# Performance work log

Measured on AMD Instinct MI355X. Metric: run time of the kernel, lower is better.

Reference implementation:

```python
import jax, jax.numpy as jnp
import numpy as np

D_MODEL = 1024
N_HEADS = 16
D_K = D_MODEL // N_HEADS

def setup_inputs() -> dict:
    key = jax.random.key(0)
    ks = jax.random.split(key, 11)
    B, S = 2, 2048
    s = 1.0 / np.sqrt(D_MODEL)
    inp = {
        'Q': jax.random.normal(ks[0], (B, S, D_MODEL), jnp.float32),
        'K': jax.random.normal(ks[1], (B, S, D_MODEL), jnp.float32),
        'V': jax.random.normal(ks[2], (B, S, D_MODEL), jnp.float32),
        'Wq': jax.random.normal(ks[3], (D_MODEL, D_MODEL), jnp.float32) * s,
        'bq': jnp.zeros((D_MODEL,), jnp.float32),
        'Wk': jax.random.normal(ks[4], (D_MODEL, D_MODEL), jnp.float32) * s,
        'bk': jnp.zeros((D_MODEL,), jnp.float32),
        'Wv': jax.random.normal(ks[5], (D_MODEL, D_MODEL), jnp.float32) * s,
        'bv': jnp.zeros((D_MODEL,), jnp.float32),
        'Wo': jax.random.normal(ks[6], (D_MODEL, D_MODEL), jnp.float32) * s,
        'bo': jnp.zeros((D_MODEL,), jnp.float32),
    }
    return inp

def _split_heads(x):
    B, S, _ = x.shape
    return x.reshape(B, S, N_HEADS, D_K).transpose(0, 2, 1, 3)  # [B,H,S,dk]

def reference(Q, K, V, Wq, bq, Wk, bk, Wv, bv, Wo, bo):
    q = _split_heads(Q @ Wq.T + bq)
    k = _split_heads(K @ Wk.T + bk)
    v = _split_heads(V @ Wv.T + bv)
    scores = jnp.einsum('bhqd,bhkd->bhqk', q, k) / jnp.sqrt(jnp.asarray(D_K, q.dtype))
    attn_weights = jax.nn.softmax(scores, axis=-1)          # [B,H,S,S]
    attn_out = jnp.einsum('bhqk,bhkd->bhqd', attn_weights, v)
    B, H, S, dk = attn_out.shape
    attn_out = attn_out.transpose(0, 2, 1, 3).reshape(B, S, H * dk)
    out = attn_out @ Wo.T + bo
    return (out, attn_weights)
```

## Files before the change

kernel.cpp:

```cpp
#include <hip/hip_runtime.h>
#include <hip/hip_bf16.h>
#include <math.h>


typedef __bf16 bf16;
typedef __bf16 bf16x8 __attribute__((ext_vector_type(8)));
typedef float  f32x4  __attribute__((ext_vector_type(4)));

#define GLDS16(gp, lp) __builtin_amdgcn_global_load_lds(                     \
    (const __attribute__((address_space(1))) void*)(gp),                     \
    (__attribute__((address_space(3))) void*)(lp), 16, 0, 0)

#define QSCALE 0.18033688011112042f

static __device__ __forceinline__ bf16x8 cvt8(const f32x4 lo, const f32x4 hi) {
    bf16x8 r;
    r[0] = (bf16)lo[0]; r[1] = (bf16)lo[1]; r[2] = (bf16)lo[2]; r[3] = (bf16)lo[3];
    r[4] = (bf16)hi[0]; r[5] = (bf16)hi[1]; r[6] = (bf16)hi[2]; r[7] = (bf16)hi[3];
    return r;
}

__global__ __launch_bounds__(256)
void cvt7(const float* __restrict__ s0, const float* __restrict__ s1, const float* __restrict__ s2,
          const float* __restrict__ s3, const float* __restrict__ s4, const float* __restrict__ s5,
          const float* __restrict__ s6,
          bf16* __restrict__ d0, bf16* __restrict__ d1, bf16* __restrict__ d2,
          bf16* __restrict__ d3, bf16* __restrict__ d4, bf16* __restrict__ d5,
          bf16* __restrict__ d6)
{
    const int seg = blockIdx.y;
    const float* s; bf16* d; int n;
    switch (seg) {
        case 0: s = s0; d = d0; n = 4194304; break;
        case 1: s = s1; d = d1; n = 4194304; break;
        case 2: s = s2; d = d2; n = 4194304; break;
        case 3: s = s3; d = d3; n = 1048576; break;
        case 4: s = s4; d = d4; n = 1048576; break;
        case 5: s = s5; d = d5; n = 1048576; break;
        default: s = s6; d = d6; n = 1048576; break;
    }
    const size_t i = ((size_t)blockIdx.x * 256 + threadIdx.x) * 8;
    if (i >= (size_t)n) return;
    const f32x4 lo = *(const f32x4*)(s + i);
    const f32x4 hi = *(const f32x4*)(s + i + 4);
    *(bf16x8*)(d + i) = cvt8(lo, hi);
}

template<int MODE>
__global__ __launch_bounds__(256)
void gemm_bb(const bf16* __restrict__ A0, const bf16* __restrict__ A1, const bf16* __restrict__ A2,
             const bf16* __restrict__ W0, const bf16* __restrict__ W1, const bf16* __restrict__ W2,
             const float* __restrict__ B0, const float* __restrict__ B1, const float* __restrict__ B2,
             void* __restrict__ O0v, void* __restrict__ O1v, void* __restrict__ O2v)
{
    __shared__ __align__(16) bf16 As[128 * 32];
    __shared__ __align__(16) bf16 Bs[128 * 32];

    const int tid  = threadIdx.x;
    const int lane = tid & 63;
    const int w    = tid >> 6;
    const int wr   = w >> 1, wc = w & 1;
    const int g    = lane >> 4, c = lane & 15;

    const int mb  = blockIdx.x, nb = blockIdx.y;
    const int mat = (MODE == 1) ? (nb >> 3) : 0;
    const int nbi = (MODE == 1) ? (nb & 7) : nb;

    const bf16*  A  = (MODE == 1) ? (mat == 0 ? A0 : (mat == 1 ? A1 : A2)) : A0;
    const bf16*  W  = (MODE == 1) ? (mat == 0 ? W0 : (mat == 1 ? W1 : W2)) : W0;
    const float* Bi = (MODE == 1) ? (mat == 0 ? B0 : (mat == 1 ? B1 : B2)) : B0;

    const size_t m0 = (size_t)mb * 128;
    const int    n0 = nbi * 128;

    f32x4 acc[4][4];
#pragma unroll
    for (int i = 0; i < 4; i++)
#pragma unroll
        for (int j = 0; j < 4; j++) acc[i][j] = (f32x4){0.f, 0.f, 0.f, 0.f};

    const int srow = lane >> 2;
    const int spos = lane & 3;

    for (int k0 = 0; k0 < 1024; k0 += 32) {
        __syncthreads();
#pragma unroll
        for (int s = 0; s < 2; s++) {
            const int ca  = w * 2 + s;
            const int row = ca * 16 + srow;
            GLDS16(A + (size_t)(m0 + row) * 1024 + k0 + ((spos ^ ((row >> 1) & 3)) << 3),
                   &As[ca * 512]);
            GLDS16(W + (size_t)(n0 + row) * 1024 + k0 + ((spos ^ ((row >> 1) & 3)) << 3),
                   &Bs[ca * 512]);
        }
        __syncthreads();

        bf16x8 av[4], bv[4];
#pragma unroll
        for (int i = 0; i < 4; i++) {
            const int row = wr * 64 + i * 16 + c;
            av[i] = *(const bf16x8*)&As[row * 32 + ((g ^ ((row >> 1) & 3)) << 3)];
        }
#pragma unroll
        for (int j = 0; j < 4; j++) {
            const int row = wc * 64 + j * 16 + c;
            bv[j] = *(const bf16x8*)&Bs[row * 32 + ((g ^ ((row >> 1) & 3)) << 3)];
        }
#pragma unroll
        for (int i = 0; i < 4; i++)
#pragma unroll
            for (int j = 0; j < 4; j++)
                acc[i][j] = __builtin_amdgcn_mfma_f32_16x16x32_bf16(av[i], bv[j], acc[i][j], 0, 0, 0);
    }

    const float scl = (MODE == 1 && mat == 0) ? QSCALE : 1.0f;
#pragma unroll
    for (int j = 0; j < 4; j++) {
        const int   nl   = wc * 64 + j * 16 + c;
        const int   n    = n0 + nl;
        const float bval = Bi[n];
#pragma unroll
        for (int i = 0; i < 4; i++) {
#pragma unroll
            for (int r = 0; r < 4; r++) {
                const size_t m   = m0 + wr * 64 + i * 16 + g * 4 + r;
                const float  val = (acc[i][j][r] + bval) * scl;
                if (MODE == 0) {
                    ((float*)O0v)[m * 1024 + n] = val;
                } else {
                    const bf16 ob = (bf16)val;
                    const int  bb = (int)(m >> 11), s = (int)(m & 2047);
                    const int  hh = n >> 6, d = n & 63;
                    if (mat < 2) {
                        bf16* Oqk = (mat == 0) ? (bf16*)O0v : (bf16*)O1v;
                        Oqk[(((size_t)bb * 16 + hh) * 2048 + s) * 64 + d] = ob;
                    } else {
                        ((bf16*)O2v)[(((size_t)bb * 16 + hh) * 64 + d) * 2048 + s] = ob;
                    }
                }
            }
        }
    }
}

template<int MODE>
__global__ __launch_bounds__(256)
void gemm_n64(const bf16* __restrict__ A0, const bf16* __restrict__ W0,
              const float* __restrict__ B0, void* __restrict__ O0v)
{
    __shared__ __align__(16) bf16 As[128 * 32];
    __shared__ __align__(16) bf16 Bs[64 * 32];

    const int tid  = threadIdx.x;
    const int lane = tid & 63;
    const int w    = tid >> 6;
    const int wr   = w >> 1, wc = w & 1;
    const int g    = lane >> 4, c = lane & 15;

    const int mb = blockIdx.x, nbi = blockIdx.y;

    const size_t m0 = (size_t)mb * 128;
    const int    n0 = nbi * 64;

    f32x4 acc[4][2];
#pragma unroll
    for (int i = 0; i < 4; i++)
#pragma unroll
        for (int j = 0; j < 2; j++) acc[i][j] = (f32x4){0.f, 0.f, 0.f, 0.f};

    const int srow = lane >> 2;
    const int spos = lane & 3;

    for (int k0 = 0; k0 < 1024; k0 += 32) {
        __syncthreads();
#pragma unroll
        for (int s = 0; s < 2; s++) {
            const int ca  = w * 2 + s;
            const int row = ca * 16 + srow;
            GLDS16(A0 + (size_t)(m0 + row) * 1024 + k0 + ((spos ^ ((row >> 1) & 3)) << 3),
                   &As[ca * 512]);
        }
        {
            const int row = w * 16 + srow;
            GLDS16(W0 + (size_t)(n0 + row) * 1024 + k0 + ((spos ^ ((row >> 1) & 3)) << 3),
                   &Bs[w * 512]);
        }
        __syncthreads();

        bf16x8 av[4], bv[2];
#pragma unroll
        for (int i = 0; i < 4; i++) {
            const int row = wr * 64 + i * 16 + c;
            av[i] = *(const bf16x8*)&As[row * 32 + ((g ^ ((row >> 1) & 3)) << 3)];
        }
#pragma unroll
        for (int j = 0; j < 2; j++) {
            const int row = wc * 32 + j * 16 + c;
            bv[j] = *(const bf16x8*)&Bs[row * 32 + ((g ^ ((row >> 1) & 3)) << 3)];
        }
#pragma unroll
        for (int i = 0; i < 4; i++)
#pragma unroll
            for (int j = 0; j < 2; j++)
                acc[i][j] = __builtin_amdgcn_mfma_f32_16x16x32_bf16(av[i], bv[j], acc[i][j], 0, 0, 0);
    }

#pragma unroll
    for (int j = 0; j < 2; j++) {
        const int   nl   = wc * 32 + j * 16 + c;
        const int   n    = n0 + nl;
        const float bval = B0[n];
#pragma unroll
        for (int i = 0; i < 4; i++) {
#pragma unroll
            for (int r = 0; r < 4; r++) {
                const size_t m = m0 + wr * 64 + i * 16 + g * 4 + r;
                ((float*)O0v)[m * 1024 + n] = acc[i][j][r] + bval;
            }
        }
    }
}

template<int MODE>
__global__ __launch_bounds__(256)
void gemm_bt(const void* __restrict__ A0v, const void* __restrict__ A1v, const void* __restrict__ A2v,
             const float* __restrict__ W0, const float* __restrict__ W1, const float* __restrict__ W2,
             const float* __restrict__ B0, const float* __restrict__ B1, const float* __restrict__ B2,
             void* __restrict__ O0v, void* __restrict__ O1v, void* __restrict__ O2v)
{
    __shared__ __align__(16) float AsF[128 * 32];
    __shared__ __align__(16) float BsF[128 * 32];
    bf16* AsH = (bf16*)AsF;

    const int tid  = threadIdx.x;
    const int lane = tid & 63;
    const int w    = tid >> 6;
    const int wr   = w >> 1, wc = w & 1;
    const int g    = lane >> 4, c = lane & 15;

    const int mb  = blockIdx.x, nb = blockIdx.y;
    const int mat = (MODE == 1) ? (nb >> 3) : 0;
    const int nbi = (MODE == 1) ? (nb & 7) : nb;

    const float* Af = (MODE == 1)
        ? (mat == 0 ? (const float*)A0v : (mat == 1 ? (const float*)A1v : (const float*)A2v))
        : nullptr;
    const bf16*  Ah = (MODE == 0) ? (const bf16*)A0v : nullptr;
    const float* W  = (MODE == 1) ? (mat == 0 ? W0 : (mat == 1 ? W1 : W2)) : W0;
    const float* Bi = (MODE == 1) ? (mat == 0 ? B0 : (mat == 1 ? B1 : B2)) : B0;

    const size_t m0 = (size_t)mb * 128;
    const int    n0 = nbi * 128;

    f32x4 acc[4][4];
#pragma unroll
    for (int i = 0; i < 4; i++)
#pragma unroll
        for (int j = 0; j < 4; j++) acc[i][j] = (f32x4){0.f, 0.f, 0.f, 0.f};

    for (int k0 = 0; k0 < 1024; k0 += 32) {
        __syncthreads();
        if constexpr (MODE == 1) {
#pragma unroll
            for (int s = 0; s < 4; s++) {
                const int ca  = w * 4 + s;
                const int row = ca * 8 + (lane >> 3);
                const int pos = lane & 7;
                GLDS16(Af + (size_t)(m0 + row) * 1024 + k0 + ((pos ^ (row & 7)) << 2), &AsF[ca * 256]);
            }
        } else {
#pragma unroll
            for (int s = 0; s < 2; s++) {
                const int ca  = w * 2 + s;
                const int row = ca * 16 + (lane >> 2);
                const int pos = lane & 3;
                GLDS16(Ah + (size_t)(m0 + row) * 1024 + k0 + ((pos ^ ((row >> 1) & 3)) << 3), &AsH[ca * 512]);
            }
        }
#pragma unroll
        for (int s = 0; s < 4; s++) {
            const int cb  = w * 4 + s;
            const int row = cb * 8 + (lane >> 3);
            const int pos = lane & 7;
            GLDS16(W + (size_t)(n0 + row) * 1024 + k0 + ((pos ^ (row & 7)) << 2), &BsF[cb * 256]);
        }
        __syncthreads();

        bf16x8 av[4], bv[4];
#pragma unroll
        for (int i = 0; i < 4; i++) {
            const int row = wr * 64 + i * 16 + c;
            if constexpr (MODE == 1) {
                const int s7 = row & 7;
                const f32x4 lo = *(const f32x4*)&AsF[row * 32 + (((2 * g)     ^ s7) << 2)];
                const f32x4 hi = *(const f32x4*)&AsF[row * 32 + (((2 * g + 1) ^ s7) << 2)];
                av[i] = cvt8(lo, hi);
            } else {
                av[i] = *(const bf16x8*)&AsH[row * 32 + ((g ^ ((row >> 1) & 3)) << 3)];
            }
        }
#pragma unroll
        for (int j = 0; j < 4; j++) {
            const int row = wc * 64 + j * 16 + c;
            const int s7  = row & 7;
            const f32x4 lo = *(const f32x4*)&BsF[row * 32 + (((2 * g)     ^ s7) << 2)];
            const f32x4 hi = *(const f32x4*)&BsF[row * 32 + (((2 * g + 1) ^ s7) << 2)];
            bv[j] = cvt8(lo, hi);
        }
#pragma unroll
        for (int i = 0; i < 4; i++)
#pragma unroll
            for (int j = 0; j < 4; j++)
                acc[i][j] = __builtin_amdgcn_mfma_f32_16x16x32_bf16(av[i], bv[j], acc[i][j], 0, 0, 0);
    }

    const float scl = (MODE == 1 && mat == 0) ? QSCALE : 1.0f;
#pragma unroll
    for (int j = 0; j < 4; j++) {
        const int   nl   = wc * 64 + j * 16 + c;
        const int   n    = n0 + nl;
        const float bval = Bi[n];
#pragma unroll
        for (int i = 0; i < 4; i++) {
#pragma unroll
            for (int r = 0; r < 4; r++) {
                const size_t m   = m0 + wr * 64 + i * 16 + g * 4 + r;
                const float  val = (acc[i][j][r] + bval) * scl;
                if (MODE == 0) {
                    ((float*)O0v)[m * 1024 + n] = val;
                } else {
                    const bf16 ob = (bf16)val;
                    const int  bb = (int)(m >> 11), s = (int)(m & 2047);
                    const int  hh = n >> 6, d = n & 63;
                    if (mat < 2) {
                        bf16* Oqk = (mat == 0) ? (bf16*)O0v : (bf16*)O1v;
                        Oqk[(((size_t)bb * 16 + hh) * 2048 + s) * 64 + d] = ob;
                    } else {
                        ((bf16*)O2v)[(((size_t)bb * 16 + hh) * 64 + d) * 2048 + s] = ob;
                    }
                }
            }
        }
    }
}

__global__ __launch_bounds__(256, 4)
void attn_kernel(const bf16* __restrict__ Qh, const bf16* __restrict__ Kh,
                 const bf16* __restrict__ VhT, float* __restrict__ PW,
                 bf16* __restrict__ AO)
{
    __shared__ __align__(16) bf16 Ks[2 * 64 * 64];
    __shared__ __align__(16) bf16 Vs[2 * 64 * 64];
    __shared__ __align__(16) bf16 Ps[64 * 64];

    const int tid  = threadIdx.x;
    const int lane = tid & 63;
    const int w    = tid >> 6;
    const int g    = lane >> 4, c = lane & 15;

    const int L   = blockIdx.x;
    const int swz = (L & 7) * 128 + (L >> 3);
    const int bh  = swz >> 5;
    const int qb  = swz & 31;

    const bf16* qp = Qh + (((size_t)bh * 2048) + qb * 64) * 64;
    const bf16* kp = Kh + ((size_t)bh * 2048) * 64;
    const bf16* vp = VhT + ((size_t)bh * 64) * 2048;
    float*      pw = PW + (size_t)bh * 2048 * 2048 + (size_t)(qb * 64) * 2048;

    bf16x8 aq[2];
#pragma unroll
    for (int kk = 0; kk < 2; kk++)
        aq[kk] = *(const bf16x8*)(qp + (w * 16 + c) * 64 + kk * 32 + g * 8);

    const int srow = (lane >> 3);
    const int spos = lane & 7;

    float lr[4] = {0.f, 0.f, 0.f, 0.f};
#pragma unroll
    for (int s2 = 0; s2 < 2; s2++) {
        const int cs = w * 2 + s2, row = cs * 8 + srow;
        GLDS16(kp + (size_t)row * 64 + ((spos ^ (row & 7)) << 3), &Ks[cs * 512]);
    }
    asm volatile("s_waitcnt vmcnt(0)" ::: "memory");
    __builtin_amdgcn_s_barrier();
    asm volatile("" ::: "memory");

    for (int t = 0; t < 32; t++) {
        const bf16* kb = &Ks[(t & 1) * 4096];
        if (t < 31) {
#pragma unroll
            for (int s2 = 0; s2 < 2; s2++) {
                const int cs = w * 2 + s2, row = cs * 8 + srow;
                GLDS16(kp + (size_t)((t + 1) * 64 + row) * 64 + ((spos ^ (row & 7)) << 3),
                       &Ks[((t + 1) & 1) * 4096 + cs * 512]);
            }
        }
        f32x4 sj[4];
#pragma unroll
        for (int j = 0; j < 4; j++) sj[j] = (f32x4){0.f, 0.f, 0.f, 0.f};
#pragma unroll
        for (int kk = 0; kk < 2; kk++) {
#pragma unroll
            for (int j = 0; j < 4; j++) {
                const int row = j * 16 + c;
                const bf16x8 bk = *(const bf16x8*)&kb[row * 64 + (((kk * 4 + g) ^ (row & 7)) << 3)];
                sj[j] = __builtin_amdgcn_mfma_f32_16x16x32_bf16(aq[kk], bk, sj[j], 0, 0, 0);
            }
        }
#pragma unroll
        for (int r = 0; r < 4; r++)
            lr[r] += exp2f(sj[0][r]) + exp2f(sj[1][r]) + exp2f(sj[2][r]) + exp2f(sj[3][r]);

        asm volatile("s_waitcnt vmcnt(0)" ::: "memory");
        __builtin_amdgcn_s_barrier();
        asm volatile("" ::: "memory");
    }

    float inv[4];
#pragma unroll
    for (int r = 0; r < 4; r++) {
        float s = lr[r];
        s += __shfl_xor(s, 1);
        s += __shfl_xor(s, 2);
        s += __shfl_xor(s, 4);
        s += __shfl_xor(s, 8);
        inv[r] = 1.0f / s;
    }

    f32x4 oj[4];
#pragma unroll
    for (int j = 0; j < 4; j++) oj[j] = (f32x4){0.f, 0.f, 0.f, 0.f};

#pragma unroll
    for (int s2 = 0; s2 < 2; s2++) {
        const int cs = w * 2 + s2, row = cs * 8 + srow;
        GLDS16(kp + (size_t)row * 64 + ((spos ^ (row & 7)) << 3), &Ks[cs * 512]);
        GLDS16(vp + (size_t)row * 2048 + ((spos ^ (row & 7)) << 3), &Vs[cs * 512]);
    }
    asm volatile("s_waitcnt vmcnt(0)" ::: "memory");
    __builtin_amdgcn_s_barrier();
    asm volatile("" ::: "memory");

    for (int t = 0; t < 32; t++) {
        const bf16* kb = &Ks[(t & 1) * 4096];
        const bf16* vb = &Vs[(t & 1) * 4096];
        if (t < 31) {
#pragma unroll
            for (int s2 = 0; s2 < 2; s2++) {
                const int cs = w * 2 + s2, row = cs * 8 + srow;
                GLDS16(kp + (size_t)((t + 1) * 64 + row) * 64 + ((spos ^ (row & 7)) << 3),
                       &Ks[((t + 1) & 1) * 4096 + cs * 512]);
                GLDS16(vp + (size_t)row * 2048 + (t + 1) * 64 + ((spos ^ (row & 7)) << 3),
                       &Vs[((t + 1) & 1) * 4096 + cs * 512]);
            }
        }
        f32x4 sj[4];
#pragma unroll
        for (int j = 0; j < 4; j++) sj[j] = (f32x4){0.f, 0.f, 0.f, 0.f};
#pragma unroll
        for (int kk = 0; kk < 2; kk++) {
#pragma unroll
            for (int j = 0; j < 4; j++) {
                const int row = j * 16 + c;
                const bf16x8 bk = *(const bf16x8*)&kb[row * 64 + (((kk * 4 + g) ^ (row & 7)) << 3)];
                sj[j] = __builtin_amdgcn_mfma_f32_16x16x32_bf16(aq[kk], bk, sj[j], 0, 0, 0);
            }
        }
#pragma unroll
        for (int j = 0; j < 4; j++) {
#pragma unroll
            for (int r = 0; r < 4; r++) {
                const float p   = exp2f(sj[j][r]) * inv[r];
                const int   row = w * 16 + g * 4 + r;
                const int   col = j * 16 + c;
                __builtin_nontemporal_store(p, &pw[(size_t)row * 2048 + t * 64 + col]);
                Ps[row * 64 + (((col >> 3) ^ (row & 7)) << 3) + (col & 7)] = (bf16)p;
            }
        }
#pragma unroll
        for (int kk = 0; kk < 2; kk++) {
            const int prow = w * 16 + c;
            const bf16x8 ap = *(const bf16x8*)&Ps[prow * 64 + (((kk * 4 + g) ^ (prow & 7)) << 3)];
#pragma unroll
            for (int j = 0; j < 4; j++) {
                const int vrow = j * 16 + c;
                const bf16x8 bvv = *(const bf16x8*)&vb[vrow * 64 + (((kk * 4 + g) ^ (vrow & 7)) << 3)];
                oj[j] = __builtin_amdgcn_mfma_f32_16x16x32_bf16(ap, bvv, oj[j], 0, 0, 0);
            }
        }
        asm volatile("s_waitcnt vmcnt(16)" ::: "memory");
        __builtin_amdgcn_s_barrier();
        asm volatile("" ::: "memory");
    }

    const int b = bh >> 4, h = bh & 15;
#pragma unroll
    for (int j = 0; j < 4; j++) {
#pragma unroll
        for (int r = 0; r < 4; r++) {
            const size_t m = (size_t)b * 2048 + qb * 64 + w * 16 + g * 4 + r;
            const int    n = h * 64 + j * 16 + c;
            AO[m * 1024 + n] = (bf16)oj[j][r];
        }
    }
}

extern "C" void kernel_launch(void* const* d_in, const int* in_sizes, int n_in,
                              void* d_out, int out_size, void* d_ws, size_t ws_size,
                              hipStream_t stream)
{
    const float* Q  = (const float*)d_in[0];
    const float* K  = (const float*)d_in[1];
    const float* V  = (const float*)d_in[2];
    const float* Wq = (const float*)d_in[3];
    const float* bq = (const float*)d_in[4];
    const float* Wk = (const float*)d_in[5];
    const float* bk = (const float*)d_in[6];
    const float* Wv = (const float*)d_in[7];
    const float* bv = (const float*)d_in[8];
    const float* Wo = (const float*)d_in[9];
    const float* bo = (const float*)d_in[10];

    float* outf  = (float*)d_out;
    float* attnw = outf + (size_t)4096 * 1024;

    bf16* ws   = (bf16*)d_ws;
    bf16* qws  = ws;
    bf16* kws  = ws + 4194304;
    bf16* vws  = ws + 8388608;
    bf16* aows = ws + 12582912;

    if (ws_size >= 67108864) {
        bf16* Qb  = ws + 16777216;
        bf16* Kb  = ws + 20971520;
        bf16* Vb  = ws + 25165824;
        bf16* Wqb = ws + 29360128;
        bf16* Wkb = ws + 30408704;
        bf16* Wvb = ws + 31457280;
        bf16* Wob = ws + 32505856;

        cvt7<<<dim3(2048, 7), 256, 0, stream>>>(Q, K, V, Wq, Wk, Wv, Wo,
                                                Qb, Kb, Vb, Wqb, Wkb, Wvb, Wob);
        gemm_bb<1><<<dim3(32, 24), 256, 0, stream>>>(Qb, Kb, Vb, Wqb, Wkb, Wvb,
                                                     bq, bk, bv, qws, kws, vws);
        attn_kernel<<<dim3(1024), 256, 0, stream>>>(qws, kws, vws, attnw, aows);
        gemm_n64<0><<<dim3(32, 16), 256, 0, stream>>>(aows, Wob, bo, outf);
    } else {
        gemm_bt<1><<<dim3(32, 24), 256, 0, stream>>>(Q, K, V, Wq, Wk, Wv, bq, bk, bv, qws, kws, vws);
        attn_kernel<<<dim3(1024), 256, 0, stream>>>(qws, kws, vws, attnw, aows);
        gemm_bt<0><<<dim3(32, 8), 256, 0, stream>>>(aows, nullptr, nullptr, Wo, nullptr, nullptr,
                                                    bo, nullptr, nullptr, outf, nullptr, nullptr);
    }
}
```

Before: 272.8 us.

## Process 128 query rows per attention block to reuse K/V tiles

Each attention block now handles 128 query rows instead of 64, with each wave computing two 16-row groups against every loaded K and V tile. This halves the grid size and halves K/V LDS traffic per query row, and the P tile buffer is doubled. The cost is more registers per thread (launch bounds lowered to 3 waves) and fewer blocks to spread across CUs, which may hurt latency hiding for the dominant attention-weight stores.

```diff
diff --git a/kernel.cpp b/kernel.cpp
--- a/kernel.cpp
+++ b/kernel.cpp
@@ -344,14 +344,14 @@
     }
 }
 
-__global__ __launch_bounds__(256, 4)
+__global__ __launch_bounds__(256, 3)
 void attn_kernel(const bf16* __restrict__ Qh, const bf16* __restrict__ Kh,
                  const bf16* __restrict__ VhT, float* __restrict__ PW,
                  bf16* __restrict__ AO)
 {
     __shared__ __align__(16) bf16 Ks[2 * 64 * 64];
     __shared__ __align__(16) bf16 Vs[2 * 64 * 64];
-    __shared__ __align__(16) bf16 Ps[64 * 64];
+    __shared__ __align__(16) bf16 Ps[128 * 64];
 
     const int tid  = threadIdx.x;
     const int lane = tid & 63;
@@ -359,24 +359,26 @@
     const int g    = lane >> 4, c = lane & 15;
 
     const int L   = blockIdx.x;
-    const int swz = (L & 7) * 128 + (L >> 3);
-    const int bh  = swz >> 5;
-    const int qb  = swz & 31;
-
-    const bf16* qp = Qh + (((size_t)bh * 2048) + qb * 64) * 64;
+    const int swz = (L & 7) * 64 + (L >> 3);
+    const int bh  = swz >> 4;
+    const int qb  = swz & 15;
+
+    const bf16* qp = Qh + (((size_t)bh * 2048) + qb * 128) * 64;
     const bf16* kp = Kh + ((size_t)bh * 2048) * 64;
     const bf16* vp = VhT + ((size_t)bh * 64) * 2048;
-    float*      pw = PW + (size_t)bh * 2048 * 2048 + (size_t)(qb * 64) * 2048;
-
-    bf16x8 aq[2];
-#pragma unroll
-    for (int kk = 0; kk < 2; kk++)
-        aq[kk] = *(const bf16x8*)(qp + (w * 16 + c) * 64 + kk * 32 + g * 8);
+    float*      pw = PW + (size_t)bh * 2048 * 2048 + (size_t)(qb * 128) * 2048;
+
+    bf16x8 aq[2][2];
+#pragma unroll
+    for (int rg = 0; rg < 2; rg++)
+#pragma unroll
+        for (int kk = 0; kk < 2; kk++)
+            aq[rg][kk] = *(const bf16x8*)(qp + (w * 32 + rg * 16 + c) * 64 + kk * 32 + g * 8);
 
     const int srow = (lane >> 3);
     const int spos = lane & 7;
 
-    float lr[4] = {0.f, 0.f, 0.f, 0.f};
+    float lr[2][4] = {{0.f,0.f,0.f,0.f},{0.f,0.f,0.f,0.f}};
 #pragma unroll
     for (int s2 = 0; s2 < 2; s2++) {
         const int cs = w * 2 + s2, row = cs * 8 + srow;
@@ -396,41 +398,51 @@
                        &Ks[((t + 1) & 1) * 4096 + cs * 512]);
             }
         }
-        f32x4 sj[4];
-#pragma unroll
-        for (int j = 0; j < 4; j++) sj[j] = (f32x4){0.f, 0.f, 0.f, 0.f};
+        f32x4 sj[2][4];
+#pragma unroll
+        for (int rg = 0; rg < 2; rg++)
+#pragma unroll
+            for (int j = 0; j < 4; j++) sj[rg][j] = (f32x4){0.f, 0.f, 0.f, 0.f};
 #pragma unroll
         for (int kk = 0; kk < 2; kk++) {
 #pragma unroll
             for (int j = 0; j < 4; j++) {
                 const int row = j * 16 + c;
                 const bf16x8 bk = *(const bf16x8*)&kb[row * 64 + (((kk * 4 + g) ^ (row & 7)) << 3)];
-                sj[j] = __builtin_amdgcn_mfma_f32_16x16x32_bf16(aq[kk], bk, sj[j], 0, 0, 0);
-            }
-        }
-#pragma unroll
-        for (int r = 0; r < 4; r++)
-            lr[r] += exp2f(sj[0][r]) + exp2f(sj[1][r]) + exp2f(sj[2][r]) + exp2f(sj[3][r]);
+                sj[0][j] = __builtin_amdgcn_mfma_f32_16x16x32_bf16(aq[0][kk], bk, sj[0][j], 0, 0, 0);
+                sj[1][j] = __builtin_amdgcn_mfma_f32_16x16x32_bf16(aq[1][kk], bk, sj[1][j], 0, 0, 0);
+            }
+        }
+#pragma unroll
+        for (int rg = 0; rg < 2; rg++)
+#pragma unroll
+            for (int r = 0; r < 4; r++)
+                lr[rg][r] += exp2f(sj[rg][0][r]) + exp2f(sj[rg][1][r])
+                           + exp2f(sj[rg][2][r]) + exp2f(sj[rg][3][r]);
 
         asm volatile("s_waitcnt vmcnt(0)" ::: "memory");
         __builtin_amdgcn_s_barrier();
         asm volatile("" ::: "memory");
     }
 
-    float inv[4];
-#pragma unroll
-    for (int r = 0; r < 4; r++) {
-        float s = lr[r];
-        s += __shfl_xor(s, 1);
-        s += __shfl_xor(s, 2);
-        s += __shfl_xor(s, 4);
-        s += __shfl_xor(s, 8);
-        inv[r] = 1.0f / s;
-    }
-
-    f32x4 oj[4];
-#pragma unroll
-    for (int j = 0; j < 4; j++) oj[j] = (f32x4){0.f, 0.f, 0.f, 0.f};
+    float inv[2][4];
+#pragma unroll
+    for (int rg = 0; rg < 2; rg++)
+#pragma unroll
+        for (int r = 0; r < 4; r++) {
+            float s = lr[rg][r];
+            s += __shfl_xor(s, 1);
+            s += __shfl_xor(s, 2);
+            s += __shfl_xor(s, 4);
+            s += __shfl_xor(s, 8);
+            inv[rg][r] = 1.0f / s;
+        }
+
+    f32x4 oj[2][4];
+#pragma unroll
+    for (int rg = 0; rg < 2; rg++)
+#pragma unroll
+        for (int j = 0; j < 4; j++) oj[rg][j] = (f32x4){0.f, 0.f, 0.f, 0.f};
 
 #pragma unroll
     for (int s2 = 0; s2 < 2; s2++) {
@@ -455,53 +467,65 @@
                        &Vs[((t + 1) & 1) * 4096 + cs * 512]);
             }
         }
-        f32x4 sj[4];
-#pragma unroll
-        for (int j = 0; j < 4; j++) sj[j] = (f32x4){0.f, 0.f, 0.f, 0.f};
+        f32x4 sj[2][4];
+#pragma unroll
+        for (int rg = 0; rg < 2; rg++)
+#pragma unroll
+            for (int j = 0; j < 4; j++) sj[rg][j] = (f32x4){0.f, 0.f, 0.f, 0.f};
 #pragma unroll
         for (int kk = 0; kk < 2; kk++) {
 #pragma unroll
             for (int j = 0; j < 4; j++) {
                 const int row = j * 16 + c;
                 const bf16x8 bk = *(const bf16x8*)&kb[row * 64 + (((kk * 4 + g) ^ (row & 7)) << 3)];
-                sj[j] = __builtin_amdgcn_mfma_f32_16x16x32_bf16(aq[kk], bk, sj[j], 0, 0, 0);
-            }
-        }
-#pragma unroll
-        for (int j = 0; j < 4; j++) {
-#pragma unroll
-            for (int r = 0; r < 4; r++) {
-                const float p   = exp2f(sj[j][r]) * inv[r];
-                const int   row = w * 16 + g * 4 + r;
-                const int   col = j * 16 + c;
-                __builtin_nontemporal_store(p, &pw[(size_t)row * 2048 + t * 64 + col]);
-                Ps[row * 64 + (((col >> 3) ^ (row & 7)) << 3) + (col & 7)] = (bf16)p;
+                sj[0][j] = __builtin_amdgcn_mfma_f32_16x16x32_bf16(aq[0][kk], bk, sj[0][j], 0, 0, 0);
+                sj[1][j] = __builtin_amdgcn_mfma_f32_16x16x32_bf16(aq[1][kk], bk, sj[1][j], 0, 0, 0);
+            }
+        }
+#pragma unroll
+        for (int rg = 0; rg < 2; rg++) {
+#pragma unroll
+            for (int j = 0; j < 4; j++) {
+#pragma unroll
+                for (int r = 0; r < 4; r++) {
+                    const float p   = exp2f(sj[rg][j][r]) * inv[rg][r];
+                    const int   row = w * 32 + rg * 16 + g * 4 + r;
+                    const int   col = j * 16 + c;
+                    __builtin_nontemporal_store(p, &pw[(size_t)row * 2048 + t * 64 + col]);
+                    Ps[row * 64 + (((col >> 3) ^ (row & 7)) << 3) + (col & 7)] = (bf16)p;
+                }
             }
         }
 #pragma unroll
         for (int kk = 0; kk < 2; kk++) {
-            const int prow = w * 16 + c;
-            const bf16x8 ap = *(const bf16x8*)&Ps[prow * 64 + (((kk * 4 + g) ^ (prow & 7)) << 3)];
+            const int p0 = w * 32 + c;
+            const int p1 = w * 32 + 16 + c;
+            const bf16x8 ap0 = *(const bf16x8*)&Ps[p0 * 64 + (((kk * 4 + g) ^ (p0 & 7)) << 3)];
+            const bf16x8 ap1 = *(const bf16x8*)&Ps[p1 * 64 + (((kk * 4 + g) ^ (p1 & 7)) << 3)];
 #pragma unroll
             for (int j = 0; j < 4; j++) {
                 const int vrow = j * 16 + c;
                 const bf16x8 bvv = *(const bf16x8*)&vb[vrow * 64 + (((kk * 4 + g) ^ (vrow & 7)) << 3)];
-                oj[j] = __builtin_amdgcn_mfma_f32_16x16x32_bf16(ap, bvv, oj[j], 0, 0, 0);
-            }
-        }
-        asm volatile("s_waitcnt vmcnt(16)" ::: "memory");
+                oj[0][j] = __builtin_amdgcn_mfma_f32_16x16x32_bf16(ap0, bvv, oj[0][j], 0, 0, 0);
+                oj[1][j] = __builtin_amdgcn_mfma_f32_16x16x32_bf16(ap1, bvv, oj[1][j], 0, 0, 0);
+            }
+        }
+        asm volatile("s_waitcnt vmcnt(32)" ::: "memory");
         __builtin_amdgcn_s_barrier();
         asm volatile("" ::: "memory");
     }
 
     const int b = bh >> 4, h = bh & 15;
 #pragma unroll
-    for (int j = 0; j < 4; j++) {
-#pragma unroll
-        for (int r = 0; r < 4; r++) {
-            const size_t m = (size_t)b * 2048 + qb * 64 + w * 16 + g * 4 + r;
-            const int    n = h * 64 + j * 16 + c;
-            AO[m * 1024 + n] = (bf16)oj[j][r];
+    for (int rg = 0; rg < 2; rg++) {
+#pragma unroll
+        for (int j = 0; j < 4; j++) {
+#pragma unroll
+            for (int r = 0; r < 4; r++) {
+                const size_t m = (size_t)b * 2048 + qb * 128 + w * 32 + rg * 16 + g * 4 + r;
+                const int    n = h * 64 + j * 16 + c;
+                AO[m * 1024 + n] = (bf16)oj[rg][j][r];
+            }
         }
     }
 }
@@ -544,11 +568,11 @@
                                                 Qb, Kb, Vb, Wqb, Wkb, Wvb, Wob);
         gemm_bb<1><<<dim3(32, 24), 256, 0, stream>>>(Qb, Kb, Vb, Wqb, Wkb, Wvb,
                                                      bq, bk, bv, qws, kws, vws);
-        attn_kernel<<<dim3(1024), 256, 0, stream>>>(qws, kws, vws, attnw, aows);
+        attn_kernel<<<dim3(512), 256, 0, stream>>>(qws, kws, vws, attnw, aows);
         gemm_n64<0><<<dim3(32, 16), 256, 0, stream>>>(aows, Wob, bo, outf);
     } else {
         gemm_bt<1><<<dim3(32, 24), 256, 0, stream>>>(Q, K, V, Wq, Wk, Wv, bq, bk, bv, qws, kws, vws);
-        attn_kernel<<<dim3(1024), 256, 0, stream>>>(qws, kws, vws, attnw, aows);
+        attn_kernel<<<dim3(512), 256, 0, stream>>>(qws, kws, vws, attnw, aows);
         gemm_bt<0><<<dim3(32, 8), 256, 0, stream>>>(aows, nullptr, nullptr, Wo, nullptr, nullptr,
                                                     bo, nullptr, nullptr, outf, nullptr, nullptr);
     }
```

Result: slower. 296.5 us (+8.7%).
